# Kernel optimization log

Measured on AMD Instinct MI355X. Metric: run time of the kernel, lower is better.

## Reference

```python
import jax, jax.numpy as jnp
import numpy as np

RADIUS = 0.25
N_SAMPLE = 4096
N_NEIGHBOR = 32
OFF = 512   # voxel-coordinate offset so hashed coords are non-negative
M = 1024    # per-axis range of the voxel hash


def _bin_map():
    # 3^3 = 27 neighbor voxel offsets in {-1,0,1}^3 (Point2Voxel.extract_bin for D=3)
    g = np.stack(np.meshgrid(*([[-1, 0, 1]] * 3), indexing='ij'), -1).reshape(-1, 3)
    return jnp.asarray(g, dtype=jnp.int32)


def _hash(k):
    # k: [..., 3] int32 voxel coords -> unique int32 key (fits: 1024^3 < 2^31)
    return ((k[..., 0] + OFF) * M + (k[..., 1] + OFF)) * M + (k[..., 2] + OFF)


def setup_inputs() -> dict:
    key = jax.random.key(0)
    k1, k2 = jax.random.split(key)
    pos = jax.random.normal(k1, (8, 100000, 3), jnp.float32)
    feat = jax.random.normal(k2, (8, 100000, 64), jnp.float32)
    return {"pos": pos, "feat": feat}


def _graph_one(pos_b, rk):
    """Voxel-hash based neighbor sampling for one point cloud [N,3]."""
    N = pos_b.shape[0]
    vox = jnp.floor(pos_b / RADIUS).astype(jnp.int32)          # [N,3] voxel keys
    hkeys = _hash(vox)                                          # [N]
    order = jnp.argsort(hkeys)                                  # sort points by voxel (hash table)
    skeys = hkeys[order]
    kc, kn = jax.random.split(rk)
    centers = jax.random.randint(kc, (N_SAMPLE,), 0, N)         # sampled center point ids
    nk = _hash(vox[centers][:, None, :] + _bin_map()[None])     # [S,27] neighbor voxel keys
    lo = jnp.searchsorted(skeys, nk, side='left')               # bucket start  [S,27]
    hi = jnp.searchsorted(skeys, nk, side='right')              # bucket end    [S,27]
    counts = hi - lo                                            # bucket sizes
    cum = jnp.cumsum(counts, axis=1)                            # [S,27]
    total = cum[:, -1]                                          # candidates per center (>=1)
    # sample N_NEIGHBOR candidate slots uniformly over all neighbor-voxel points
    r = jax.random.randint(kn, (N_SAMPLE, N_NEIGHBOR), 0, 1 << 30) % total[:, None]
    slot = (r[:, :, None] >= cum[:, None, :]).sum(-1)           # which of the 27 voxels
    cum_ex = jnp.concatenate([jnp.zeros_like(cum[:, :1]), cum[:, :-1]], axis=1)
    prev = jnp.take_along_axis(cum_ex, slot, axis=1)
    start = jnp.take_along_axis(lo, slot, axis=1)
    src = order[start + (r - prev)]                             # [S,K] source point ids
    return centers, src


def reference(pos, feat):
    B, N, D = pos.shape
    C = feat.shape[-1]
    rks = jax.random.split(jax.random.key(42), B)
    centers, src = jax.vmap(_graph_one)(pos, rks)               # [B,S], [B,S,K]
    bidx = jnp.arange(B)[:, None]
    center_flag = jnp.zeros((B, N), pos.dtype).at[bidx, centers].set(1.0)
    src_flag = jnp.zeros((B, N), pos.dtype).at[bidx, src.reshape(B, -1)].set(1.0)
    b3 = jnp.arange(B)[:, None, None]
    pos_src = pos[b3, src]                                      # [B,S,K,3] gather
    pos_ctr = pos[bidx, centers]                                # [B,S,3]
    rel = pos_src - pos_ctr[:, :, None, :]                      # edge geometry
    f_src = feat[b3, src]                                       # [B,S,K,C] gather
    out = jnp.concatenate([rel, f_src], axis=-1)                # [B,S,K,3+C]
    return out, src, centers, center_flag, src_flag
```

## Files before the change

kernel.cpp:

```cpp
#include <hip/hip_runtime.h>
#include <stdint.h>

#define NB 8
#define NPTS 100000
#define NS 4096
#define NN 32
#define NCH 64
#define TLG 17
#define TSLOTS (1 << TLG)
#define TMASK (TSLOTS - 1)

#define OUT_MAIN 0ull
#define OUT_SRC  70254592ull
#define OUT_CTR  71303168ull
#define OUT_CF   71335936ull
#define OUT_SF   72135936ull

__host__ __device__ static inline uint32_t rotl32(uint32_t v, int d) {
    return (v << d) | (v >> (32 - d));
}

__host__ __device__ static inline void tf2x32(uint32_t k0, uint32_t k1,
                                              uint32_t x0, uint32_t x1,
                                              uint32_t& o0, uint32_t& o1) {
    uint32_t ks2 = k0 ^ k1 ^ 0x1BD11BDAu;
    x0 += k0; x1 += k1;
    x0 += x1; x1 = rotl32(x1, 13); x1 ^= x0;
    x0 += x1; x1 = rotl32(x1, 15); x1 ^= x0;
    x0 += x1; x1 = rotl32(x1, 26); x1 ^= x0;
    x0 += x1; x1 = rotl32(x1, 6);  x1 ^= x0;
    x0 += k1; x1 += ks2 + 1u;
    x0 += x1; x1 = rotl32(x1, 17); x1 ^= x0;
    x0 += x1; x1 = rotl32(x1, 29); x1 ^= x0;
    x0 += x1; x1 = rotl32(x1, 16); x1 ^= x0;
    x0 += x1; x1 = rotl32(x1, 24); x1 ^= x0;
    x0 += ks2; x1 += k0 + 2u;
    x0 += x1; x1 = rotl32(x1, 13); x1 ^= x0;
    x0 += x1; x1 = rotl32(x1, 15); x1 ^= x0;
    x0 += x1; x1 = rotl32(x1, 26); x1 ^= x0;
    x0 += x1; x1 = rotl32(x1, 6);  x1 ^= x0;
    x0 += k0; x1 += k1 + 3u;
    x0 += x1; x1 = rotl32(x1, 17); x1 ^= x0;
    x0 += x1; x1 = rotl32(x1, 29); x1 ^= x0;
    x0 += x1; x1 = rotl32(x1, 16); x1 ^= x0;
    x0 += x1; x1 = rotl32(x1, 24); x1 ^= x0;
    x0 += k1; x1 += ks2 + 4u;
    x0 += x1; x1 = rotl32(x1, 13); x1 ^= x0;
    x0 += x1; x1 = rotl32(x1, 15); x1 ^= x0;
    x0 += x1; x1 = rotl32(x1, 26); x1 ^= x0;
    x0 += x1; x1 = rotl32(x1, 6);  x1 ^= x0;
    x0 += ks2; x1 += k0 + 5u;
    o0 = x0; o1 = x1;
}

struct RngKeys {
    uint32_t c0[NB], c1[NB];
    uint32_t n0[NB], n1[NB];
};

__device__ static inline uint32_t pbits32(uint32_t k0, uint32_t k1, uint32_t u) {
    uint32_t o0, o1;
    tf2x32(k0, k1, 0u, u, o0, o1);
    return o0 ^ o1;
}

__device__ static inline int voxhash(const float* __restrict__ p) {
    int vx = (int)floorf(p[0] * 4.0f);
    int vy = (int)floorf(p[1] * 4.0f);
    int vz = (int)floorf(p[2] * 4.0f);
    return ((vx + 512) << 20) | ((vy + 512) << 10) | (vz + 512);
}

__device__ static inline int hslot(int hk) {
    return (int)(((uint32_t)hk * 2654435761u) >> (32 - TLG)) & TMASK;
}

__device__ static inline int probe_find(const int* __restrict__ key, int base, int hk) {
    int slot = hslot(hk);
    while (key[base + slot] != hk) slot = (slot + 1) & TMASK;
    return slot;
}

__global__ void k_insert(const float* __restrict__ pos,
                         int* __restrict__ tab_key, int* __restrict__ tab_cnt) {
    int t = blockIdx.x * blockDim.x + threadIdx.x;
    int b = t / NPTS;
    int hk = voxhash(pos + (size_t)t * 3);
    int base = b << TLG;
    int slot = hslot(hk);
    while (true) {
        int prev = atomicCAS(&tab_key[base + slot], -1, hk);
        if (prev == -1 || prev == hk) break;
        slot = (slot + 1) & TMASK;
    }
    atomicAdd(&tab_cnt[base + slot], 1);
}

__global__ void k_starts(int* __restrict__ tab_cnt, int* __restrict__ tab_start,
                         int* __restrict__ bctr) {
    __shared__ int sdata[256];
    __shared__ int sbase;
    int t = blockIdx.x * blockDim.x + threadIdx.x;
    int tid = threadIdx.x;
    int b = t >> TLG;
    int c = tab_cnt[t];
    sdata[tid] = c;
    __syncthreads();
    for (int off = 1; off < 256; off <<= 1) {
        int x = (tid >= off) ? sdata[tid - off] : 0;
        __syncthreads();
        sdata[tid] += x;
        __syncthreads();
    }
    if (tid == 255) sbase = atomicAdd(&bctr[b], sdata[255]);
    __syncthreads();
    if (c > 0) {
        tab_start[t] = sbase + sdata[tid] - c;
        tab_cnt[t] = 0;
    }
}

__global__ void k_scatter(const float* __restrict__ pos,
                          const int* __restrict__ tab_key, int* __restrict__ tab_cnt,
                          const int* __restrict__ tab_start, int* __restrict__ listA) {
    int t = blockIdx.x * blockDim.x + threadIdx.x;
    int b = t / NPTS, i = t - b * NPTS;
    int hk = voxhash(pos + (size_t)t * 3);
    int base = b << TLG;
    int slot = probe_find(tab_key, base, hk);
    int a = atomicAdd(&tab_cnt[base + slot], 1);
    listA[(size_t)b * NPTS + tab_start[base + slot] + a] = i;
}

__global__ void k_rank(const float* __restrict__ pos,
                       const int* __restrict__ tab_key, const int* __restrict__ tab_cnt,
                       const int* __restrict__ tab_start,
                       const int* __restrict__ listA, int* __restrict__ listB) {
    int t = blockIdx.x * blockDim.x + threadIdx.x;
    int b = t / NPTS, i = t - b * NPTS;
    int hk = voxhash(pos + (size_t)t * 3);
    int base = b << TLG;
    int slot = probe_find(tab_key, base, hk);
    int s0 = tab_start[base + slot];
    int c = tab_cnt[base + slot];
    const int* L = listA + (size_t)b * NPTS + s0;
    int rank = 0;
    for (int k = 0; k < c; k++) rank += (L[k] < i) ? 1 : 0;
    listB[(size_t)b * NPTS + s0 + rank] = i;
}

__global__ void k_centers(RngKeys keys, const float* __restrict__ pos,
                          int* __restrict__ centers_ws, int* __restrict__ ctrhk_ws,
                          float* __restrict__ out_ctr, float* __restrict__ out_cf) {
    int t = blockIdx.x * blockDim.x + threadIdx.x;
    int b = t / NS, s = t - b * NS;
    uint32_t lower = pbits32(keys.c0[b], keys.c1[b], (uint32_t)s);
    int c = (int)(lower % 100000u);
    centers_ws[t] = c;
    ctrhk_ws[t] = voxhash(pos + ((size_t)b * NPTS + c) * 3);
    out_ctr[t] = (float)c;
    out_cf[(size_t)b * NPTS + c] = 1.0f;
}

__global__ void k_bins(const int* __restrict__ tab_key, const int* __restrict__ tab_cnt,
                       const int* __restrict__ tab_start, const int* __restrict__ ctrhk_ws,
                       int* __restrict__ lo_ws, int* __restrict__ cnt_ws) {
    int t = blockIdx.x * blockDim.x + threadIdx.x;
    int bin = t % 27;
    int bs = t / 27;
    int b = bs / NS;
    int hk = ctrhk_ws[bs] + ((bin / 9) - 1) * (1 << 20)
                          + (((bin / 3) % 3) - 1) * (1 << 10)
                          + ((bin % 3) - 1);
    int base = b << TLG;
    int slot = hslot(hk);
    int lo = 0, c = 0;
    while (true) {
        int k = tab_key[base + slot];
        if (k == hk) { lo = tab_start[base + slot]; c = tab_cnt[base + slot]; break; }
        if (k == -1) break;
        slot = (slot + 1) & TMASK;
    }
    lo_ws[t] = lo;
    cnt_ws[t] = c;
}

__global__ void k_cum(int* __restrict__ cnt_cum) {
    int t = blockIdx.x * blockDim.x + threadIdx.x;
    int acc = 0;
    int* a = cnt_cum + (size_t)t * 27;
    for (int i = 0; i < 27; i++) { acc += a[i]; a[i] = acc; }
}

__global__ void k_select(RngKeys keys, const int* __restrict__ listB,
                         const int* __restrict__ lo_ws, const int* __restrict__ cum_ws,
                         int* __restrict__ src_ws,
                         float* __restrict__ out_src, float* __restrict__ out_sf) {
    int t = blockIdx.x * blockDim.x + threadIdx.x;
    int b = t >> 17;
    int u = t & (NS * NN - 1);
    uint32_t lower = pbits32(keys.n0[b], keys.n1[b], (uint32_t)u);
    int bs = b * NS + (u >> 5);
    const int* cum = cum_ws + (size_t)bs * 27;
    int total = cum[26];
    int r = (int)(lower & 0x3FFFFFFFu) % total;
    int slot = 0, prev = 0;
    #pragma unroll
    for (int i = 0; i < 27; i++) {
        int ci = cum[i];
        if (r >= ci) { slot = i + 1; prev = ci; }
    }
    int pos_in = lo_ws[(size_t)bs * 27 + slot] + (r - prev);
    int src = listB[(size_t)b * NPTS + pos_in];
    src_ws[t] = src;
    out_src[t] = (float)src;
    out_sf[(size_t)b * NPTS + src] = 1.0f;
}

__global__ void k_gather(const float* __restrict__ pos, const float* __restrict__ feat,
                         const int* __restrict__ centers_ws, const int* __restrict__ src_ws,
                         float* __restrict__ out) {
    __shared__ float sbuf[16 * 67];
    int t = threadIdx.x;
    int g = t >> 4, q = t & 15;
    long long row0 = (long long)blockIdx.x * 16;
    long long row = row0 + g;
    int b = (int)(row >> 17);
    int u = (int)(row & (NS * NN - 1));
    int s = u >> 5;
    int src = src_ws[row];
    const float4 fv = *(const float4*)(feat + ((size_t)b * NPTS + src) * NCH + 4 * q);
    float* sb = sbuf + g * 67;
    sb[3 + 4 * q + 0] = fv.x;
    sb[3 + 4 * q + 1] = fv.y;
    sb[3 + 4 * q + 2] = fv.z;
    sb[3 + 4 * q + 3] = fv.w;
    if (q < 3) {
        int ctr = centers_ws[b * NS + s];
        sb[q] = pos[((size_t)b * NPTS + src) * 3 + q]
              - pos[((size_t)b * NPTS + ctr) * 3 + q];
    }
    __syncthreads();
    float4* ob = (float4*)(out + (size_t)row0 * 67);
    const float4* sv = (const float4*)sbuf;
    ob[t] = sv[t];
    if (t < 12) ob[256 + t] = sv[256 + t];
}

extern "C" void kernel_launch(void* const* d_in, const int* in_sizes, int n_in,
                              void* d_out, int out_size, void* d_ws, size_t ws_size,
                              hipStream_t stream) {
    (void)in_sizes; (void)n_in; (void)out_size; (void)ws_size;
    const float* pos = (const float*)d_in[0];
    const float* feat = (const float*)d_in[1];
    float* out = (float*)d_out;

    RngKeys keys;
    for (int b = 0; b < NB; b++) {
        uint32_t rk0, rk1, kc0, kc1, kn0, kn1;
        tf2x32(0u, 42u, 0u, (uint32_t)b, rk0, rk1);
        tf2x32(rk0, rk1, 0u, 0u, kc0, kc1);
        tf2x32(rk0, rk1, 0u, 1u, kn0, kn1);
        tf2x32(kc0, kc1, 0u, 1u, keys.c0[b], keys.c1[b]);
        tf2x32(kn0, kn1, 0u, 1u, keys.n0[b], keys.n1[b]);
    }

    int* tab_key    = (int*)d_ws;
    int* tab_cnt    = tab_key + (size_t)NB * TSLOTS;
    int* bctr       = tab_cnt + (size_t)NB * TSLOTS;
    int* tab_start  = bctr + NB;
    int* listA      = tab_start + (size_t)NB * TSLOTS;
    int* listB      = listA + (size_t)NB * NPTS;
    int* lo_ws      = listB + (size_t)NB * NPTS;
    int* cum_ws     = lo_ws + (size_t)NB * NS * 27;
    int* centers_ws = cum_ws + (size_t)NB * NS * 27;
    int* ctrhk_ws   = centers_ws + (size_t)NB * NS;
    int* src_ws     = ctrhk_ws + (size_t)NB * NS;

    hipMemsetAsync(tab_key, 0xFF, (size_t)NB * TSLOTS * 4, stream);
    hipMemsetAsync(tab_cnt, 0, ((size_t)NB * TSLOTS + NB) * 4, stream);
    hipMemsetAsync((char*)d_out + OUT_CF * 4, 0, (size_t)(2 * NB * NPTS) * 4, stream);

    k_insert <<<(NB * NPTS) / 256, 256, 0, stream>>>(pos, tab_key, tab_cnt);
    k_starts <<<(NB * TSLOTS) / 256, 256, 0, stream>>>(tab_cnt, tab_start, bctr);
    k_scatter<<<(NB * NPTS) / 256, 256, 0, stream>>>(pos, tab_key, tab_cnt, tab_start, listA);
    k_rank   <<<(NB * NPTS) / 256, 256, 0, stream>>>(pos, tab_key, tab_cnt, tab_start,
                                                     listA, listB);
    k_centers<<<(NB * NS) / 256, 256, 0, stream>>>(keys, pos, centers_ws, ctrhk_ws,
                                                   out + OUT_CTR, out + OUT_CF);
    k_bins   <<<(NB * NS * 27) / 256, 256, 0, stream>>>(tab_key, tab_cnt, tab_start,
                                                        ctrhk_ws, lo_ws, cum_ws);
    k_cum    <<<(NB * NS) / 256, 256, 0, stream>>>(cum_ws);
    k_select <<<(NB * NS * NN) / 256, 256, 0, stream>>>(keys, listB, lo_ws, cum_ws,
                                                        src_ws, out + OUT_SRC, out + OUT_SF);
    k_gather <<<(NB * NS * NN) / 16, 256, 0, stream>>>(pos, feat, centers_ws, src_ws, out);
}
```

Baseline: 436.0 us.

## Cache hash slots per point, fuse center/bin and cumsum/select kernels, replace memsets

Insert now records each point's hash-table slot, so the scatter and rank kernels no longer recompute voxel hashes or re-probe the table. Center sampling is folded into the bin-lookup kernel, and the per-center prefix sum is folded into neighbor selection using shared memory. Three memsets are replaced by one zeroing kernel. Together this cuts kernel launches and redundant global traffic, at the cost of an extra slot array in workspace and duplicated RNG/hash work across the 27 bin threads.

```diff
diff --git a/kernel.cpp b/kernel.cpp
--- a/kernel.cpp
+++ b/kernel.cpp
@@ -75,14 +75,18 @@
     return (int)(((uint32_t)hk * 2654435761u) >> (32 - TLG)) & TMASK;
 }
 
-__device__ static inline int probe_find(const int* __restrict__ key, int base, int hk) {
-    int slot = hslot(hk);
-    while (key[base + slot] != hk) slot = (slot + 1) & TMASK;
-    return slot;
+__global__ void k_zero(int* __restrict__ tab_key, int* __restrict__ tab_cnt,
+                       int* __restrict__ bctr, float4* __restrict__ flags4) {
+    int t = blockIdx.x * blockDim.x + threadIdx.x;
+    tab_key[t] = -1;
+    tab_cnt[t] = 0;
+    if (t < (2 * NB * NPTS) / 4) flags4[t] = make_float4(0.f, 0.f, 0.f, 0.f);
+    if (t < NB) bctr[t] = 0;
 }
 
 __global__ void k_insert(const float* __restrict__ pos,
-                         int* __restrict__ tab_key, int* __restrict__ tab_cnt) {
+                         int* __restrict__ tab_key, int* __restrict__ tab_cnt,
+                         int* __restrict__ slotOf) {
     int t = blockIdx.x * blockDim.x + threadIdx.x;
     int b = t / NPTS;
     int hk = voxhash(pos + (size_t)t * 3);
@@ -93,6 +97,7 @@
         if (prev == -1 || prev == hk) break;
         slot = (slot + 1) & TMASK;
     }
+    slotOf[t] = slot;
     atomicAdd(&tab_cnt[base + slot], 1);
 }
 
@@ -120,88 +125,87 @@
     }
 }
 
-__global__ void k_scatter(const float* __restrict__ pos,
-                          const int* __restrict__ tab_key, int* __restrict__ tab_cnt,
+__global__ void k_scatter(const int* __restrict__ slotOf, int* __restrict__ tab_cnt,
                           const int* __restrict__ tab_start, int* __restrict__ listA) {
     int t = blockIdx.x * blockDim.x + threadIdx.x;
     int b = t / NPTS, i = t - b * NPTS;
-    int hk = voxhash(pos + (size_t)t * 3);
-    int base = b << TLG;
-    int slot = probe_find(tab_key, base, hk);
-    int a = atomicAdd(&tab_cnt[base + slot], 1);
-    listA[(size_t)b * NPTS + tab_start[base + slot] + a] = i;
-}
-
-__global__ void k_rank(const float* __restrict__ pos,
-                       const int* __restrict__ tab_key, const int* __restrict__ tab_cnt,
-                       const int* __restrict__ tab_start,
+    int slot = (b << TLG) + slotOf[t];
+    int a = atomicAdd(&tab_cnt[slot], 1);
+    listA[(size_t)b * NPTS + tab_start[slot] + a] = i;
+}
+
+__global__ void k_rank(const int* __restrict__ slotOf,
+                       const int* __restrict__ tab_cnt, const int* __restrict__ tab_start,
                        const int* __restrict__ listA, int* __restrict__ listB) {
     int t = blockIdx.x * blockDim.x + threadIdx.x;
     int b = t / NPTS, i = t - b * NPTS;
-    int hk = voxhash(pos + (size_t)t * 3);
-    int base = b << TLG;
-    int slot = probe_find(tab_key, base, hk);
-    int s0 = tab_start[base + slot];
-    int c = tab_cnt[base + slot];
+    int slot = (b << TLG) + slotOf[t];
+    int s0 = tab_start[slot];
+    int c = tab_cnt[slot];
     const int* L = listA + (size_t)b * NPTS + s0;
     int rank = 0;
     for (int k = 0; k < c; k++) rank += (L[k] < i) ? 1 : 0;
     listB[(size_t)b * NPTS + s0 + rank] = i;
 }
 
-__global__ void k_centers(RngKeys keys, const float* __restrict__ pos,
-                          int* __restrict__ centers_ws, int* __restrict__ ctrhk_ws,
-                          float* __restrict__ out_ctr, float* __restrict__ out_cf) {
-    int t = blockIdx.x * blockDim.x + threadIdx.x;
-    int b = t / NS, s = t - b * NS;
+__global__ void k_binsel(RngKeys keys, const float* __restrict__ pos,
+                         const int* __restrict__ tab_key, const int* __restrict__ tab_cnt,
+                         const int* __restrict__ tab_start,
+                         int* __restrict__ centers_ws,
+                         int* __restrict__ lo_ws, int* __restrict__ cnt_ws,
+                         float* __restrict__ out_ctr, float* __restrict__ out_cf) {
+    int t = blockIdx.x * blockDim.x + threadIdx.x;
+    int bin = t % 27;
+    int bs = t / 27;
+    int b = bs >> 12, s = bs & (NS - 1);
     uint32_t lower = pbits32(keys.c0[b], keys.c1[b], (uint32_t)s);
     int c = (int)(lower % 100000u);
-    centers_ws[t] = c;
-    ctrhk_ws[t] = voxhash(pos + ((size_t)b * NPTS + c) * 3);
-    out_ctr[t] = (float)c;
-    out_cf[(size_t)b * NPTS + c] = 1.0f;
-}
-
-__global__ void k_bins(const int* __restrict__ tab_key, const int* __restrict__ tab_cnt,
-                       const int* __restrict__ tab_start, const int* __restrict__ ctrhk_ws,
-                       int* __restrict__ lo_ws, int* __restrict__ cnt_ws) {
-    int t = blockIdx.x * blockDim.x + threadIdx.x;
-    int bin = t % 27;
-    int bs = t / 27;
-    int b = bs / NS;
-    int hk = ctrhk_ws[bs] + ((bin / 9) - 1) * (1 << 20)
-                          + (((bin / 3) % 3) - 1) * (1 << 10)
-                          + ((bin % 3) - 1);
+    const float* p = pos + ((size_t)b * NPTS + c) * 3;
+    int hk = voxhash(p) + ((bin / 9) - 1) * (1 << 20)
+                        + (((bin / 3) % 3) - 1) * (1 << 10)
+                        + ((bin % 3) - 1);
     int base = b << TLG;
     int slot = hslot(hk);
-    int lo = 0, c = 0;
+    int lo = 0, cnt = 0;
     while (true) {
         int k = tab_key[base + slot];
-        if (k == hk) { lo = tab_start[base + slot]; c = tab_cnt[base + slot]; break; }
+        if (k == hk) { lo = tab_start[base + slot]; cnt = tab_cnt[base + slot]; break; }
         if (k == -1) break;
         slot = (slot + 1) & TMASK;
     }
     lo_ws[t] = lo;
-    cnt_ws[t] = c;
-}
-
-__global__ void k_cum(int* __restrict__ cnt_cum) {
-    int t = blockIdx.x * blockDim.x + threadIdx.x;
-    int acc = 0;
-    int* a = cnt_cum + (size_t)t * 27;
-    for (int i = 0; i < 27; i++) { acc += a[i]; a[i] = acc; }
-}
-
-__global__ void k_select(RngKeys keys, const int* __restrict__ listB,
-                         const int* __restrict__ lo_ws, const int* __restrict__ cum_ws,
+    cnt_ws[t] = cnt;
+    if (bin == 13) {
+        centers_ws[bs] = c;
+        out_ctr[bs] = (float)c;
+        out_cf[(size_t)b * NPTS + c] = 1.0f;
+    }
+}
+
+__global__ void k_cumsel(RngKeys keys, const int* __restrict__ listB,
+                         const int* __restrict__ lo_ws, const int* __restrict__ cnt_ws,
                          int* __restrict__ src_ws,
                          float* __restrict__ out_src, float* __restrict__ out_sf) {
-    int t = blockIdx.x * blockDim.x + threadIdx.x;
-    int b = t >> 17;
-    int u = t & (NS * NN - 1);
-    uint32_t lower = pbits32(keys.n0[b], keys.n1[b], (uint32_t)u);
-    int bs = b * NS + (u >> 5);
-    const int* cum = cum_ws + (size_t)bs * 27;
+    __shared__ int scnt[216];
+    __shared__ int slo[216];
+    int tid = threadIdx.x;
+    int base216 = blockIdx.x * 216;
+    if (tid < 216) {
+        scnt[tid] = cnt_ws[base216 + tid];
+        slo[tid]  = lo_ws[base216 + tid];
+    }
+    __syncthreads();
+    if (tid < 8) {
+        int* a = scnt + tid * 27;
+        int acc = 0;
+        for (int i = 0; i < 27; i++) { acc += a[i]; a[i] = acc; }
+    }
+    __syncthreads();
+    int g = tid >> 5, n = tid & 31;
+    int bs = blockIdx.x * 8 + g;
+    int b = bs >> 12, s = bs & (NS - 1);
+    uint32_t lower = pbits32(keys.n0[b], keys.n1[b], (uint32_t)(s * NN + n));
+    const int* cum = scnt + g * 27;
     int total = cum[26];
     int r = (int)(lower & 0x3FFFFFFFu) % total;
     int slot = 0, prev = 0;
@@ -210,10 +214,11 @@
         int ci = cum[i];
         if (r >= ci) { slot = i + 1; prev = ci; }
     }
-    int pos_in = lo_ws[(size_t)bs * 27 + slot] + (r - prev);
+    int pos_in = slo[g * 27 + slot] + (r - prev);
     int src = listB[(size_t)b * NPTS + pos_in];
-    src_ws[t] = src;
-    out_src[t] = (float)src;
+    int oi = bs * NN + n;
+    src_ws[oi] = src;
+    out_src[oi] = (float)src;
     out_sf[(size_t)b * NPTS + src] = 1.0f;
 }
 
@@ -267,31 +272,28 @@
 
     int* tab_key    = (int*)d_ws;
     int* tab_cnt    = tab_key + (size_t)NB * TSLOTS;
-    int* bctr       = tab_cnt + (size_t)NB * TSLOTS;
-    int* tab_start  = bctr + NB;
-    int* listA      = tab_start + (size_t)NB * TSLOTS;
+    int* tab_start  = tab_cnt + (size_t)NB * TSLOTS;
+    int* bctr       = tab_start + (size_t)NB * TSLOTS;
+    int* slotOf     = bctr + NB;
+    int* listA      = slotOf + (size_t)NB * NPTS;
     int* listB      = listA + (size_t)NB * NPTS;
     int* lo_ws      = listB + (size_t)NB * NPTS;
-    int* cum_ws     = lo_ws + (size_t)NB * NS * 27;
-    int* centers_ws = cum_ws + (size_t)NB * NS * 27;
-    int* ctrhk_ws   = centers_ws + (size_t)NB * NS;
-    int* src_ws     = ctrhk_ws + (size_t)NB * NS;
-
-    hipMemsetAsync(tab_key, 0xFF, (size_t)NB * TSLOTS * 4, stream);
-    hipMemsetAsync(tab_cnt, 0, ((size_t)NB * TSLOTS + NB) * 4, stream);
-    hipMemsetAsync((char*)d_out + OUT_CF * 4, 0, (size_t)(2 * NB * NPTS) * 4, stream);
-
-    k_insert <<<(NB * NPTS) / 256, 256, 0, stream>>>(pos, tab_key, tab_cnt);
+    int* cnt_ws     = lo_ws + (size_t)NB * NS * 27;
+    int* centers_ws = cnt_ws + (size_t)NB * NS * 27;
+    int* src_ws     = centers_ws + (size_t)NB * NS;
+
+    k_zero   <<<(NB * TSLOTS) / 256, 256, 0, stream>>>(tab_key, tab_cnt, bctr,
+                                                       (float4*)(out + OUT_CF));
+    k_insert <<<(NB * NPTS) / 256, 256, 0, stream>>>(pos, tab_key, tab_cnt, slotOf);
     k_starts <<<(NB * TSLOTS) / 256, 256, 0, stream>>>(tab_cnt, tab_start, bctr);
-    k_scatter<<<(NB * NPTS) / 256, 256, 0, stream>>>(pos, tab_key, tab_cnt, tab_start, listA);
-    k_rank   <<<(NB * NPTS) / 256, 256, 0, stream>>>(pos, tab_key, tab_cnt, tab_start,
+    k_scatter<<<(NB * NPTS) / 256, 256, 0, stream>>>(slotOf, tab_cnt, tab_start, listA);
+    k_rank   <<<(NB * NPTS) / 256, 256, 0, stream>>>(slotOf, tab_cnt, tab_start,
                                                      listA, listB);
-    k_centers<<<(NB * NS) / 256, 256, 0, stream>>>(keys, pos, centers_ws, ctrhk_ws,
-                                                   out + OUT_CTR, out + OUT_CF);
-    k_bins   <<<(NB * NS * 27) / 256, 256, 0, stream>>>(tab_key, tab_cnt, tab_start,
-                                                        ctrhk_ws, lo_ws, cum_ws);
-    k_cum    <<<(NB * NS) / 256, 256, 0, stream>>>(cum_ws);
-    k_select <<<(NB * NS * NN) / 256, 256, 0, stream>>>(keys, listB, lo_ws, cum_ws,
-                                                        src_ws, out + OUT_SRC, out + OUT_SF);
+    k_binsel <<<(NB * NS * 27) / 256, 256, 0, stream>>>(keys, pos, tab_key, tab_cnt,
+                                                        tab_start, centers_ws,
+                                                        lo_ws, cnt_ws,
+                                                        out + OUT_CTR, out + OUT_CF);
+    k_cumsel <<<(NB * NS) / 8, 256, 0, stream>>>(keys, listB, lo_ws, cnt_ws,
+                                                 src_ws, out + OUT_SRC, out + OUT_SF);
     k_gather <<<(NB * NS * NN) / 16, 256, 0, stream>>>(pos, feat, centers_ws, src_ws, out);
 }
```

Result: faster. 417.0 us (-4.4%).
